# Optimization experiments

Hardware: AMD Instinct MI355X
Metric: run time of the kernel (lower is better)

The kernel has to match this reference:

```python
import jax, jax.numpy as jnp
import numpy as np

BS9 = 9
NA9 = BS9 * BS9  # 81


def _make_windows():
    """All 5-in-a-row windows on a 9x9 board, as flat cell indices. (140, 5)."""
    wins = []
    for dr, dc in ((0, 1), (1, 0), (1, 1), (1, -1)):
        for r in range(BS9):
            for c in range(BS9):
                er, ec = r + 4 * dr, c + 4 * dc
                if 0 <= er < BS9 and 0 <= ec < BS9:
                    wins.append([(r + k * dr) * BS9 + (c + k * dc) for k in range(5)])
    return np.asarray(wins, dtype=np.int32)

_W_NP = _make_windows()                      # (140, 5)
_M_NP = np.zeros((NA9, _W_NP.shape[0]), dtype=np.int32)
for w in range(_W_NP.shape[0]):
    _M_NP[_W_NP[w], w] = 1                   # MEMBER[idx, w] = 1 iff cell idx is in window w

WINDOWS = jnp.asarray(_W_NP)                 # (140, 5)
MEMBER = jnp.asarray(_M_NP)                  # (81, 140)
# score table indexed by stone count 0..5 (pc>=5 clamps to 5 since window len is 5)
TABLE = jnp.asarray([0.0, 5.0, 50.0, 500.0, 5000.0, 100000.0], dtype=jnp.float32)


def setup_inputs() -> dict:
    key = jax.random.key(0)
    k1, k2 = jax.random.split(key)
    B = 2048
    boards = jax.random.randint(k1, (B, NA9), 0, 3).astype(jnp.float32)   # cells in {0,1,2}
    current_player = jax.random.randint(k2, (B,), 1, 3).astype(jnp.int32) # {1,2}
    return {"boards": boards, "current_player": current_player}


def reference(boards, current_player):
    # boards: (B, 81) float32 with values {0,1,2}; current_player: (B,) int32 {1,2}
    player = current_player.astype(boards.dtype)[:, None, None]  # (B,1,1)
    opp = 3.0 - player
    cells = boards[:, WINDOWS]                                    # (B,140,5)
    pc = jnp.sum(cells == player, axis=-1)                        # (B,140) player count per window
    oc = jnp.sum(cells == opp, axis=-1)                           # (B,140) opponent count

    # static eval of the current board (used for the value head)
    plus = jnp.where((oc == 0) & (pc > 0), TABLE[pc], 0.0)
    minus = jnp.where((pc == 0) & (oc > 0), TABLE[oc], 0.0)
    ev = jnp.sum(plus - minus, axis=-1)                           # (B,)

    # 1-ply lookahead: placing player's stone at empty cell idx adds MEMBER[idx] to pc
    pc_new = pc[:, None, :] + MEMBER[None]                        # (B,81,140)
    win = jnp.any((MEMBER[None] == 1) & (pc_new == 5), axis=-1)   # (B,81)
    ocb = oc[:, None, :]
    plus_n = jnp.where((ocb == 0) & (pc_new > 0), TABLE[pc_new], 0.0)
    minus_n = jnp.where((pc_new == 0) & (ocb > 0), TABLE[ocb], 0.0)
    score = jnp.sum(plus_n - minus_n, axis=-1)                    # (B,81)

    empty = boards == 0                                           # (B,81)
    logits = jnp.where(empty, jnp.where(win, 100000.0, score), -1000000.0)
    policy = jax.nn.softmax(logits * 0.03, axis=-1)               # (B,81)
    value = jnp.clip(jnp.tanh(ev / 3000.0), -0.95, 0.95)[:, None] # (B,1)
    return policy, value
```

## Files before the change

### kernel.cpp

```cpp
#include <hip/hip_runtime.h>
#include <math.h>

#define NB 81
#define NW 140

__device__ __constant__ float TBL[6] = {0.f, 5.f, 50.f, 500.f, 5000.f, 100000.f};

__device__ __forceinline__ int imax(int a, int b) { return a > b ? a : b; }
__device__ __forceinline__ int imin(int a, int b) { return a < b ? a : b; }

__device__ __forceinline__ float wave_sum(float v) {
#pragma unroll
    for (int m = 1; m < 64; m <<= 1) v += __shfl_xor(v, m, 64);
    return v;
}
__device__ __forceinline__ float wave_max(float v) {
#pragma unroll
    for (int m = 1; m < 64; m <<= 1) v = fmaxf(v, __shfl_xor(v, m, 64));
    return v;
}

__device__ __forceinline__ float cell_logit(int a, const int* bd, const unsigned* pw, float ev) {
    if (bd[a] != 0) return -1000000.0f;
    const int r = a / 9, c = a - 9 * (a / 9);
    float delta = 0.f;
    bool win = false;
    auto acc = [&](int w) {
        const unsigned v = pw[w];
        const int pc = (int)(v & 0xffu);
        const int oc = (int)(v >> 8);
        win |= (pc == 4);
        int pcn = pc + 1; if (pcn > 5) pcn = 5;
        if (oc == 0)      delta += TBL[pcn] - TBL[pc];
        else if (pc == 0) delta += TBL[oc];
    };
    int lo, hi;
    lo = imax(0, c - 4); hi = imin(c, 4);
    for (int c0 = lo; c0 <= hi; ++c0) acc(r * 5 + c0);
    lo = imax(0, r - 4); hi = imin(r, 4);
    for (int r0 = lo; r0 <= hi; ++r0) acc(45 + r0 * 9 + c);
    lo = imax(0, imax(r - 4, c - 4)); hi = imin(4, imin(r, c));
    for (int k = lo; k <= hi; ++k) acc(90 + (r - k) * 5 + (c - k));
    lo = imax(0, imax(r - 4, 4 - c)); hi = imin(4, imin(r, 8 - c));
    for (int k = lo; k <= hi; ++k) acc(115 + (r - k) * 5 + (c + k - 4));
    return win ? 100000.0f : (ev + delta);
}

__global__ __launch_bounds__(256) void heur9_kernel(const float* __restrict__ boards,
                                                    const int* __restrict__ cur,
                                                    float* __restrict__ out, int B) {
    __shared__ int sb[4][NB];
    __shared__ unsigned spw[4][NW];
    const int wave = threadIdx.x >> 6;
    const int lane = threadIdx.x & 63;
    const int b = (blockIdx.x << 2) | wave;

    int* bd = sb[wave];
    unsigned* pw = spw[wave];
    const float* brd = boards + b * NB;

    bd[lane] = (int)brd[lane];
    if (lane < NB - 64) bd[lane + 64] = (int)brd[lane + 64];
    const int player = cur[b];
    const int opp = 3 - player;
    __syncthreads();

    float evp = 0.f;
    for (int w = lane; w < NW; w += 64) {
        int base, stride;
        if (w < 45)       { const int r = w / 5;        base = r * 9 + (w - r * 5);              stride = 1;  }
        else if (w < 90)  { const int t = w - 45, r0 = t / 9;  base = r0 * 9 + (t - r0 * 9);     stride = 9;  }
        else if (w < 115) { const int t = w - 90, r0 = t / 5;  base = r0 * 9 + (t - r0 * 5);     stride = 10; }
        else              { const int t = w - 115, r0 = t / 5; base = r0 * 9 + (t - r0 * 5) + 4; stride = 8;  }
        int pc = 0, oc = 0;
#pragma unroll
        for (int k = 0; k < 5; ++k) {
            const int v = bd[base + k * stride];
            pc += (v == player);
            oc += (v == opp);
        }
        pw[w] = (unsigned)(pc | (oc << 8));
        if (oc == 0)      evp += TBL[pc];
        else if (pc == 0) evp -= TBL[oc];
    }
    const float ev = wave_sum(evp);
    __syncthreads();

    const float l1 = cell_logit(lane, bd, pw, ev) * 0.03f;
    const float l2 = (lane < NB - 64) ? cell_logit(lane + 64, bd, pw, ev) * 0.03f : -INFINITY;

    const float m = wave_max(fmaxf(l1, l2));
    const float e1 = __expf(l1 - m);
    const float e2 = (lane < NB - 64) ? __expf(l2 - m) : 0.f;
    const float inv = 1.0f / wave_sum(e1 + e2);

    out[b * NB + lane] = e1 * inv;
    if (lane < NB - 64) out[b * NB + lane + 64] = e2 * inv;
    if (lane == 0) {
        const float v = tanhf(ev * (1.f / 3000.f));
        out[B * NB + b] = fminf(fmaxf(v, -0.95f), 0.95f);
    }
}

extern "C" void kernel_launch(void* const* d_in, const int* in_sizes, int n_in,
                              void* d_out, int out_size, void* d_ws, size_t ws_size,
                              hipStream_t stream) {
    const float* boards = (const float*)d_in[0];
    const int* cur = (const int*)d_in[1];
    float* out = (float*)d_out;
    const int B = in_sizes[0] / NB;
    const int blocks = B / 4;
    heur9_kernel<<<blocks, 256, 0, stream>>>(boards, cur, out, B);
}
```

Measured before the change: 65.20 us.

## Use ballot bitboards with popcount window counts and precomputed per-window deltas

Board occupancy is now built as 64-bit ballot bitmasks for player and opponent. Window counts come from popcounts against constexpr window masks held in constant memory, which replaces the strided LDS reads of the board. Each window's score delta (or a large win sentinel) is precomputed into shared memory, and each cell sums its windows through a packed constant-memory index table instead of running branchy loop bounds. The cost is a larger constant table with divergent constant accesses, plus a sentinel threshold used to detect wins.

```diff
diff --git a/kernel.cpp b/kernel.cpp
--- a/kernel.cpp
+++ b/kernel.cpp
@@ -4,10 +4,42 @@
 #define NB 81
 #define NW 140
 
-__device__ __constant__ float TBL[6] = {0.f, 5.f, 50.f, 500.f, 5000.f, 100000.f};
+struct Tables {
+    unsigned long long mlo[NW];
+    unsigned long long mhi[NW];
+    unsigned cw32[NB][5];
+};
 
-__device__ __forceinline__ int imax(int a, int b) { return a > b ? a : b; }
-__device__ __forceinline__ int imin(int a, int b) { return a < b ? a : b; }
+constexpr Tables make_tables() {
+    Tables t{};
+    for (int a = 0; a < NB; ++a)
+        for (int j = 0; j < 5; ++j) t.cw32[a][j] = 0x8C8C8C8Cu;
+    int cnt[NB] = {};
+    const int DR[4] = {0, 1, 1, 1};
+    const int DC[4] = {1, 0, 1, -1};
+    int w = 0;
+    for (int d = 0; d < 4; ++d)
+        for (int r = 0; r < 9; ++r)
+            for (int c = 0; c < 9; ++c) {
+                const int er = r + 4 * DR[d], ec = c + 4 * DC[d];
+                if (er < 0 || er > 8 || ec < 0 || ec > 8) continue;
+                unsigned long long lo = 0, hi = 0;
+                for (int k = 0; k < 5; ++k) {
+                    const int cell = (r + k * DR[d]) * 9 + (c + k * DC[d]);
+                    if (cell < 64) lo |= 1ull << cell;
+                    else           hi |= 1ull << (cell - 64);
+                    const int i = cnt[cell]++;
+                    t.cw32[cell][i >> 2] &= ~(0xFFu << (8 * (i & 3)));
+                    t.cw32[cell][i >> 2] |= (unsigned)w << (8 * (i & 3));
+                }
+                t.mlo[w] = lo; t.mhi[w] = hi; ++w;
+            }
+    return t;
+}
+
+__device__ __constant__ Tables TAB = make_tables();
+__device__ __constant__ float PT[6] = {0.f, 5.f, 50.f, 500.f, 5000.f, 100000.f};
+__device__ __constant__ float DT[6] = {5.f, 45.f, 450.f, 4500.f, 95000.f, 0.f};
 
 __device__ __forceinline__ float wave_sum(float v) {
 #pragma unroll
@@ -20,74 +52,62 @@
     return v;
 }
 
-__device__ __forceinline__ float cell_logit(int a, const int* bd, const unsigned* pw, float ev) {
-    if (bd[a] != 0) return -1000000.0f;
-    const int r = a / 9, c = a - 9 * (a / 9);
-    float delta = 0.f;
-    bool win = false;
-    auto acc = [&](int w) {
-        const unsigned v = pw[w];
-        const int pc = (int)(v & 0xffu);
-        const int oc = (int)(v >> 8);
-        win |= (pc == 4);
-        int pcn = pc + 1; if (pcn > 5) pcn = 5;
-        if (oc == 0)      delta += TBL[pcn] - TBL[pc];
-        else if (pc == 0) delta += TBL[oc];
-    };
-    int lo, hi;
-    lo = imax(0, c - 4); hi = imin(c, 4);
-    for (int c0 = lo; c0 <= hi; ++c0) acc(r * 5 + c0);
-    lo = imax(0, r - 4); hi = imin(r, 4);
-    for (int r0 = lo; r0 <= hi; ++r0) acc(45 + r0 * 9 + c);
-    lo = imax(0, imax(r - 4, c - 4)); hi = imin(4, imin(r, c));
-    for (int k = lo; k <= hi; ++k) acc(90 + (r - k) * 5 + (c - k));
-    lo = imax(0, imax(r - 4, 4 - c)); hi = imin(4, imin(r, 8 - c));
-    for (int k = lo; k <= hi; ++k) acc(115 + (r - k) * 5 + (c + k - 4));
-    return win ? 100000.0f : (ev + delta);
-}
-
 __global__ __launch_bounds__(256) void heur9_kernel(const float* __restrict__ boards,
                                                     const int* __restrict__ cur,
                                                     float* __restrict__ out, int B) {
-    __shared__ int sb[4][NB];
-    __shared__ unsigned spw[4][NW];
+    __shared__ float sD[4][NW + 1];
     const int wave = threadIdx.x >> 6;
     const int lane = threadIdx.x & 63;
     const int b = (blockIdx.x << 2) | wave;
-
-    int* bd = sb[wave];
-    unsigned* pw = spw[wave];
+    float* dl = sD[wave];
     const float* brd = boards + b * NB;
 
-    bd[lane] = (int)brd[lane];
-    if (lane < NB - 64) bd[lane + 64] = (int)brd[lane + 64];
-    const int player = cur[b];
-    const int opp = 3 - player;
-    __syncthreads();
+    const float pf = (float)cur[b];
+    const float of = 3.0f - pf;
+    const float v1 = brd[lane];
+    const float v2 = (lane < NB - 64) ? brd[lane + 64] : -1.0f;
+
+    const unsigned long long p_lo = __ballot(v1 == pf);
+    const unsigned long long p_hi = __ballot((lane < NB - 64) && v2 == pf);
+    const unsigned long long o_lo = __ballot(v1 == of);
+    const unsigned long long o_hi = __ballot((lane < NB - 64) && v2 == of);
+    const unsigned long long e_lo = ~(p_lo | o_lo);
+    const unsigned long long e_hi = ~(p_hi | o_hi);
 
     float evp = 0.f;
     for (int w = lane; w < NW; w += 64) {
-        int base, stride;
-        if (w < 45)       { const int r = w / 5;        base = r * 9 + (w - r * 5);              stride = 1;  }
-        else if (w < 90)  { const int t = w - 45, r0 = t / 9;  base = r0 * 9 + (t - r0 * 9);     stride = 9;  }
-        else if (w < 115) { const int t = w - 90, r0 = t / 5;  base = r0 * 9 + (t - r0 * 5);     stride = 10; }
-        else              { const int t = w - 115, r0 = t / 5; base = r0 * 9 + (t - r0 * 5) + 4; stride = 8;  }
-        int pc = 0, oc = 0;
-#pragma unroll
-        for (int k = 0; k < 5; ++k) {
-            const int v = bd[base + k * stride];
-            pc += (v == player);
-            oc += (v == opp);
-        }
-        pw[w] = (unsigned)(pc | (oc << 8));
-        if (oc == 0)      evp += TBL[pc];
-        else if (pc == 0) evp -= TBL[oc];
+        const int pc = __popcll(p_lo & TAB.mlo[w]) + __popcll(p_hi & TAB.mhi[w]);
+        const int oc = __popcll(o_lo & TAB.mlo[w]) + __popcll(o_hi & TAB.mhi[w]);
+        float d = 0.f;
+        if (oc == 0)      { d = DT[pc]; evp += PT[pc]; }
+        else if (pc == 0) { d = PT[oc]; evp -= PT[oc]; }
+        if (pc == 4) d = 1.0e9f;
+        dl[w] = d;
     }
+    if (lane == 0) dl[NW] = 0.f;
     const float ev = wave_sum(evp);
     __syncthreads();
 
-    const float l1 = cell_logit(lane, bd, pw, ev) * 0.03f;
-    const float l2 = (lane < NB - 64) ? cell_logit(lane + 64, bd, pw, ev) * 0.03f : -INFINITY;
+    float sd1 = 0.f, sd2 = 0.f;
+#pragma unroll
+    for (int j = 0; j < 5; ++j) {
+        const unsigned q = TAB.cw32[lane][j];
+        sd1 += dl[q & 255] + dl[(q >> 8) & 255] + dl[(q >> 16) & 255] + dl[q >> 24];
+    }
+    if (lane < NB - 64) {
+#pragma unroll
+        for (int j = 0; j < 5; ++j) {
+            const unsigned q = TAB.cw32[lane + 64][j];
+            sd2 += dl[q & 255] + dl[(q >> 8) & 255] + dl[(q >> 16) & 255] + dl[q >> 24];
+        }
+    }
+    const bool emp1 = (e_lo >> lane) & 1ull;
+    const bool emp2 = (lane < NB - 64) && ((e_hi >> lane) & 1ull);
+    float l1 = emp1 ? (sd1 >= 5.0e8f ? 100000.f : ev + sd1) : -1000000.f;
+    float l2 = (lane < NB - 64)
+                 ? (emp2 ? (sd2 >= 5.0e8f ? 100000.f : ev + sd2) : -1000000.f)
+                 : -INFINITY;
+    l1 *= 0.03f; l2 *= 0.03f;
 
     const float m = wave_max(fmaxf(l1, l2));
     const float e1 = __expf(l1 - m);
@@ -109,6 +129,5 @@
     const int* cur = (const int*)d_in[1];
     float* out = (float*)d_out;
     const int B = in_sizes[0] / NB;
-    const int blocks = B / 4;
-    heur9_kernel<<<blocks, 256, 0, stream>>>(boards, cur, out, B);
+    heur9_kernel<<<B / 4, 256, 0, stream>>>(boards, cur, out, B);
 }
```

Result: faster. 57.75 us (-11.4%).
